# Kernel optimization log

Hardware: AMD Instinct MI355X
Metric: run time of the kernel (lower is better)

Reference implementation:

```python
import jax, jax.numpy as jnp
import numpy as np

B, N, C = 16, 1024, 1024
H = 16            # num_attention_heads
D = C // H        # attention_head_size = 64

def setup_inputs() -> dict:
    key = jax.random.key(0)
    k1, k2, k3 = jax.random.split(key, 3)
    scale = 1.0 / np.sqrt(C)
    return {
        "hidden_states": jax.random.normal(k1, (B, N, C), dtype=jnp.float32),
        "qkv_w": jax.random.normal(k2, (C, 3 * C), dtype=jnp.float32) * scale,
        "qkv_b": jnp.zeros((3 * C,), dtype=jnp.float32),
        "proj_w": jax.random.normal(k3, (C, C), dtype=jnp.float32) * scale,
        "proj_b": jnp.zeros((C,), dtype=jnp.float32),
    }

def reference(hidden_states, qkv_w, qkv_b, proj_w, proj_b):
    # fused QKV projection: [B, N, 3C]
    qkv = hidden_states @ qkv_w + qkv_b
    # reshape to [3, B, H, N, D]
    qkv = qkv.reshape(B, N, 3, H, D).transpose(2, 0, 3, 1, 4)
    q, k, v = qkv[0], qkv[1], qkv[2]
    # attention scores [B, H, N, N]
    scores = jnp.einsum("bhnd,bhmd->bhnm", q, k) / jnp.sqrt(jnp.float32(D))
    probs = jax.nn.softmax(scores, axis=-1)  # dropout_p=0 -> identity
    ctx = jnp.einsum("bhnm,bhmd->bhnd", probs, v)
    ctx = ctx.transpose(0, 2, 1, 3).reshape(B, N, C)
    # output projection
    return ctx @ proj_w + proj_b
```

## Files before the change

kernel.cpp:

```cpp
#include <hip/hip_runtime.h>


#define BB 16
#define NN 1024
#define CC 1024
#define HH 16
#define DD 64
#define BN (BB * NN)
#define HEADELEMS (256 * 1024 * 64)

typedef float  f4     __attribute__((ext_vector_type(4)));
typedef __bf16 bf16x8 __attribute__((ext_vector_type(8)));
typedef __bf16 bf16x4 __attribute__((ext_vector_type(4)));
typedef short  s8v    __attribute__((ext_vector_type(8)));
typedef short  s4v    __attribute__((ext_vector_type(4)));
typedef short  s2v    __attribute__((ext_vector_type(2)));

__device__ __forceinline__ short f2bf(float x) {
  union { float f; unsigned u; } a; a.f = x;
  unsigned r = a.u + 0x7fffu + ((a.u >> 16) & 1u);
  return (short)(r >> 16);
}

__device__ __forceinline__ void gl_lds16(const void* g, void* l) {
  __builtin_amdgcn_global_load_lds((__attribute__((address_space(1))) void*)g,
                                   (__attribute__((address_space(3))) void*)l,
                                   16, 0, 0);
}

__device__ __forceinline__ f4 mfma16(bf16x8 a, bf16x8 b, f4 c) {
  return __builtin_amdgcn_mfma_f32_16x16x32_bf16(a, b, c, 0, 0, 0);
}

__global__ void cast_bf16(const float* __restrict__ x, short* __restrict__ y) {
  int i = (blockIdx.x * 256 + threadIdx.x) * 4;
  float4 v = *(const float4*)&x[i];
  s4v o;
  o[0] = f2bf(v.x); o[1] = f2bf(v.y); o[2] = f2bf(v.z); o[3] = f2bf(v.w);
  *(s4v*)&y[i] = o;
}

__global__ void transpose_cast(const float* __restrict__ W, short* __restrict__ Wt,
                               int K, int Nw) {
  __shared__ float tile[32][33];
  int bx = blockIdx.x, by = blockIdx.y;
  int t = threadIdx.x;
  int tc = t & 31, tr = t >> 5;
#pragma unroll
  for (int i = 0; i < 4; ++i) {
    int r = tr + i * 8;
    tile[r][tc] = W[(size_t)(by * 32 + r) * Nw + bx * 32 + tc];
  }
  __syncthreads();
#pragma unroll
  for (int i = 0; i < 4; ++i) {
    int r = tr + i * 8;
    Wt[(size_t)(bx * 32 + r) * K + by * 32 + tc] = f2bf(tile[tc][r]);
  }
}

__global__ void transpose_v(const short* __restrict__ Vm, short* __restrict__ Vt) {
  __shared__ short tile[64][68];
  int bh = blockIdx.x, n0 = blockIdx.y * 64;
  const short* src = Vm + (size_t)bh * (NN * DD) + (size_t)n0 * DD;
  short* dst = Vt + (size_t)bh * (NN * DD) + n0;
  int t = threadIdx.x;
#pragma unroll
  for (int i2 = 0; i2 < 2; ++i2) {
    int i = t + i2 * 256;
    int r = i >> 3, c = i & 7;
    *(s8v*)&tile[r][c * 8] = *(const s8v*)&src[(size_t)r * DD + c * 8];
  }
  __syncthreads();
#pragma unroll
  for (int i2 = 0; i2 < 2; ++i2) {
    int i = t + i2 * 256;
    int d = i >> 3, c = i & 7;
    s8v v;
#pragma unroll
    for (int j = 0; j < 8; ++j) v[j] = tile[c * 8 + j][d];
    *(s8v*)&dst[(size_t)d * NN + c * 8] = v;
  }
}

template <int EPI>
__global__ __launch_bounds__(256, 2)
void gemm_bt(const short* __restrict__ A, const short* __restrict__ Bt,
             const float* __restrict__ bias, float* __restrict__ Cf,
             short* __restrict__ Cq, int M, int N, int K) {
  __shared__ short la[128 * 64];
  __shared__ short lb[128 * 64];
  const int t = threadIdx.x, lane = t & 63, w = t >> 6;
  const int row0 = blockIdx.y * 128, col0 = blockIdx.x * 128;
  const int wm = (w & 1) * 64, wn = (w >> 1) * 64;
  const int q = lane >> 4, ln = lane & 15;
  const int sr8 = lane >> 3;
  const int sc8 = (lane & 7) ^ sr8;
  f4 acc[4][4] = {};

  for (int kb = 0; kb < K; kb += 64) {
    __syncthreads();
#pragma unroll
    for (int rblk = 0; rblk < 4; ++rblk) {
      int rbase = (w * 4 + rblk) * 8;
      const short* ga = A + (size_t)(row0 + rbase + sr8) * K + kb + sc8 * 8;
      const short* gb = Bt + (size_t)(col0 + rbase + sr8) * K + kb + sc8 * 8;
      gl_lds16(ga, &la[rbase * 64]);
      gl_lds16(gb, &lb[rbase * 64]);
    }
    __syncthreads();
#pragma unroll
    for (int ks2 = 0; ks2 < 2; ++ks2) {
      const int c8 = ks2 * 4 + q;
      const int sw = (c8 ^ (ln & 7)) * 8;
      bf16x8 af[4], bfr[4];
#pragma unroll
      for (int i = 0; i < 4; ++i) {
        af[i]  = *(const bf16x8*)&la[(wm + i * 16 + ln) * 64 + sw];
        bfr[i] = *(const bf16x8*)&lb[(wn + i * 16 + ln) * 64 + sw];
      }
#pragma unroll
      for (int i = 0; i < 4; ++i)
#pragma unroll
        for (int j = 0; j < 4; ++j)
          acc[i][j] = mfma16(af[i], bfr[j], acc[i][j]);
    }
  }

#pragma unroll
  for (int i = 0; i < 4; ++i) {
    int rbase = row0 + wm + i * 16 + q * 4;
#pragma unroll
    for (int j = 0; j < 4; ++j) {
      int col = col0 + wn + j * 16 + ln;
      float bv = bias[col];
      if (EPI == 0) {
#pragma unroll
        for (int r2 = 0; r2 < 4; ++r2)
          Cf[(size_t)(rbase + r2) * N + col] = acc[i][j][r2] + bv;
      } else {
        int which = col >> 10, c = col & 1023;
        int h = c >> 6, d = c & 63;
        float scale = (which == 0) ? 0.1803368801f : 1.0f;
#pragma unroll
        for (int r2 = 0; r2 < 4; ++r2) {
          int row = rbase + r2;
          int bh = (row >> 10) * HH + h;
          size_t idx = ((size_t)bh * NN + (row & 1023)) * DD + d;
          Cq[(size_t)which * HEADELEMS + idx] = f2bf((acc[i][j][r2] + bv) * scale);
        }
      }
    }
  }
}

__global__ __launch_bounds__(512, 4)
void attn(const short* __restrict__ Qg, const short* __restrict__ Kg,
          const short* __restrict__ Vtg, short* __restrict__ ctx) {
  __shared__ short sQP[128 * 64];
  __shared__ short sK[2][64 * 64];
  __shared__ short sV[2][64 * 64];
  const int t = threadIdx.x, lane = t & 63, w = t >> 6;
  const int bh = blockIdx.x, qb = blockIdx.y;
  const short* Qh = Qg + (size_t)bh * (NN * DD) + qb * 128 * DD;
  const short* Kh = Kg + (size_t)bh * (NN * DD);
  const short* Vh = Vtg + (size_t)bh * (NN * DD);

  {
    int r0 = t >> 3, c0 = t & 7;
    gl_lds16(Qh + r0 * DD + ((c0 ^ (r0 & 7)) * 8), &sQP[t * 8]);
    int i1 = t + 512;
    int r1 = i1 >> 3, c1 = i1 & 7;
    gl_lds16(Qh + r1 * DD + ((c1 ^ (r1 & 7)) * 8), &sQP[i1 * 8]);
  }
  const int sr = t >> 3, sc = t & 7;
  const int ssc = ((sc ^ (sr & 7)) * 8);
  gl_lds16(Kh + sr * DD + ssc, &sK[0][t * 8]);
  gl_lds16(Vh + (size_t)sr * NN + ssc, &sV[0][t * 8]);

  __syncthreads();

  const int q = lane >> 4, ln = lane & 15;
  const int wq = w * 16;
  const int sw = ln & 7;

  bf16x8 qf[2];
  qf[0] = *(const bf16x8*)&sQP[(wq + ln) * 64 + ((0 + q) ^ sw) * 8];
  qf[1] = *(const bf16x8*)&sQP[(wq + ln) * 64 + ((4 + q) ^ sw) * 8];

  f4 o[4] = {};
  float lsum = 0.f;

  for (int kt = 0; kt < 16; ++kt) {
    const int cur = kt & 1;
    if (kt < 15) {
      const int nb = cur ^ 1;
      gl_lds16(Kh + (kt + 1) * 64 * DD + sr * DD + ssc, &sK[nb][t * 8]);
      gl_lds16(Vh + (size_t)sr * NN + (kt + 1) * 64 + ssc, &sV[nb][t * 8]);
    }

    f4 s[4] = {};
    __builtin_amdgcn_s_setprio(1);
#pragma unroll
    for (int ks = 0; ks < 2; ++ks) {
#pragma unroll
      for (int ki = 0; ki < 4; ++ki) {
        bf16x8 kf = *(const bf16x8*)&sK[cur][(ki * 16 + ln) * 64 + (((ks * 4 + q) ^ sw) * 8)];
        s[ki] = mfma16(kf, qf[ks], s[ki]);
      }
    }
    __builtin_amdgcn_s_setprio(0);

#pragma unroll
    for (int ki = 0; ki < 4; ++ki) {
      float p0 = exp2f(s[ki][0]), p1 = exp2f(s[ki][1]);
      float p2 = exp2f(s[ki][2]), p3 = exp2f(s[ki][3]);
      lsum += (p0 + p1) + (p2 + p3);
      bf16x4 pk;
      pk[0] = (__bf16)p0; pk[1] = (__bf16)p1;
      pk[2] = (__bf16)p2; pk[3] = (__bf16)p3;
      *(bf16x4*)&sQP[(wq + ln) * 64 + (((2 * ki + (q >> 1)) ^ sw) * 8) + (q & 1) * 4] = pk;
    }

    __builtin_amdgcn_s_setprio(1);
#pragma unroll
    for (int ks = 0; ks < 2; ++ks) {
      bf16x8 pf = *(const bf16x8*)&sQP[(wq + ln) * 64 + (((ks * 4 + q) ^ sw) * 8)];
#pragma unroll
      for (int j = 0; j < 4; ++j) {
        bf16x8 vf = *(const bf16x8*)&sV[cur][(j * 16 + ln) * 64 + (((ks * 4 + q) ^ sw) * 8)];
        o[j] = mfma16(pf, vf, o[j]);
      }
    }
    __builtin_amdgcn_s_setprio(0);

    __syncthreads();
  }

  float lfull = lsum;
  lfull += __shfl_xor(lfull, 16);
  lfull += __shfl_xor(lfull, 32);

#pragma unroll
  for (int r = 0; r < 4; ++r) {
    float lr = __shfl(lfull, q * 4 + r);
    float inv = 1.0f / lr;
    int token_row = qb * 128 + wq + q * 4 + r;
    size_t base = ((size_t)(bh >> 4) * NN + token_row) * CC + (bh & 15) * DD;
#pragma unroll
    for (int j = 0; j < 4; ++j)
      ctx[base + j * 16 + ln] = f2bf(o[j][r] * inv);
  }
}

extern "C" void kernel_launch(void* const* d_in, const int* in_sizes, int n_in,
                              void* d_out, int out_size, void* d_ws, size_t ws_size,
                              hipStream_t stream) {
  const float* hs     = (const float*)d_in[0];
  const float* qkv_w  = (const float*)d_in[1];
  const float* qkv_b  = (const float*)d_in[2];
  const float* proj_w = (const float*)d_in[3];
  const float* proj_b = (const float*)d_in[4];

  short* ws = (short*)d_ws;
  if (ws_size < 176160768ull) return;
  short* Xbf = ws;
  short* Wq  = ws + 16777216;
  short* Wp  = ws + 19922944;
  short* Qm  = ws + 20971520;
  short* Km  = ws + 37748736;
  short* Vm  = ws + 54525952;
  short* Ctx = ws + 71303168;
  short* Vt  = Xbf;

  cast_bf16<<<16384, 256, 0, stream>>>(hs, Xbf);
  transpose_cast<<<dim3(96, 32), 256, 0, stream>>>(qkv_w, Wq, 1024, 3072);
  transpose_cast<<<dim3(32, 32), 256, 0, stream>>>(proj_w, Wp, 1024, 1024);

  gemm_bt<1><<<dim3(24, 128), 256, 0, stream>>>(Xbf, Wq, qkv_b, nullptr, Qm,
                                                BN, 3 * CC, CC);
  transpose_v<<<dim3(256, 16), 256, 0, stream>>>(Vm, Vt);
  attn<<<dim3(256, 8), 512, 0, stream>>>(Qm, Km, Vt, Ctx);
  gemm_bt<0><<<dim3(8, 128), 256, 0, stream>>>(Ctx, Wp, proj_b, (float*)d_out, nullptr,
                                               BN, CC, CC);
}
```

Baseline: 420.8 us.

## Double-buffer GEMM, fuse V transpose into QKV epilogue, widen attention tiles

Measured after the change: 393.6 us. 1.07x faster.

```diff
diff --git a/kernel.cpp b/kernel.cpp
--- a/kernel.cpp
+++ b/kernel.cpp
@@ -16,6 +16,12 @@
 typedef short  s4v    __attribute__((ext_vector_type(4)));
 typedef short  s2v    __attribute__((ext_vector_type(2)));
 
+#if __has_builtin(__builtin_amdgcn_exp2f)
+#define EXP2(x) __builtin_amdgcn_exp2f(x)
+#else
+#define EXP2(x) exp2f(x)
+#endif
+
 __device__ __forceinline__ short f2bf(float x) {
   union { float f; unsigned u; } a; a.f = x;
   unsigned r = a.u + 0x7fffu + ((a.u >> 16) & 1u);
@@ -59,65 +65,51 @@
   }
 }
 
-__global__ void transpose_v(const short* __restrict__ Vm, short* __restrict__ Vt) {
-  __shared__ short tile[64][68];
-  int bh = blockIdx.x, n0 = blockIdx.y * 64;
-  const short* src = Vm + (size_t)bh * (NN * DD) + (size_t)n0 * DD;
-  short* dst = Vt + (size_t)bh * (NN * DD) + n0;
-  int t = threadIdx.x;
-#pragma unroll
-  for (int i2 = 0; i2 < 2; ++i2) {
-    int i = t + i2 * 256;
-    int r = i >> 3, c = i & 7;
-    *(s8v*)&tile[r][c * 8] = *(const s8v*)&src[(size_t)r * DD + c * 8];
-  }
-  __syncthreads();
-#pragma unroll
-  for (int i2 = 0; i2 < 2; ++i2) {
-    int i = t + i2 * 256;
-    int d = i >> 3, c = i & 7;
-    s8v v;
-#pragma unroll
-    for (int j = 0; j < 8; ++j) v[j] = tile[c * 8 + j][d];
-    *(s8v*)&dst[(size_t)d * NN + c * 8] = v;
-  }
-}
+#define GSTAGE(buf, kb)                                                        \
+  {                                                                            \
+    _Pragma("unroll")                                                          \
+    for (int rblk = 0; rblk < 4; ++rblk) {                                     \
+      int rbase = (w * 4 + rblk) * 8;                                          \
+      gl_lds16(A + (size_t)(row0 + rbase + sr8) * K + (kb) + sc8 * 8,          \
+               &la[buf][rbase * 64]);                                          \
+      gl_lds16(Bt + (size_t)(col0 + rbase + sr8) * K + (kb) + sc8 * 8,         \
+               &lb[buf][rbase * 64]);                                          \
+    }                                                                          \
+  }
 
 template <int EPI>
 __global__ __launch_bounds__(256, 2)
 void gemm_bt(const short* __restrict__ A, const short* __restrict__ Bt,
              const float* __restrict__ bias, float* __restrict__ Cf,
              short* __restrict__ Cq, int M, int N, int K) {
-  __shared__ short la[128 * 64];
-  __shared__ short lb[128 * 64];
+  __shared__ short la[2][128 * 64];
+  __shared__ short lb[2][128 * 64];
   const int t = threadIdx.x, lane = t & 63, w = t >> 6;
-  const int row0 = blockIdx.y * 128, col0 = blockIdx.x * 128;
+  int bid = blockIdx.y * gridDim.x + blockIdx.x;
+  int xcd = bid & 7, sub = bid >> 3;
+  int xg = sub >> 7, rem = sub & 127;
+  int xb = xg * 8 + (rem & 7), yb = xcd * 16 + (rem >> 3);
+  const int row0 = yb * 128, col0 = xb * 128;
   const int wm = (w & 1) * 64, wn = (w >> 1) * 64;
   const int q = lane >> 4, ln = lane & 15;
   const int sr8 = lane >> 3;
   const int sc8 = (lane & 7) ^ sr8;
   f4 acc[4][4] = {};
 
-  for (int kb = 0; kb < K; kb += 64) {
-    __syncthreads();
-#pragma unroll
-    for (int rblk = 0; rblk < 4; ++rblk) {
-      int rbase = (w * 4 + rblk) * 8;
-      const short* ga = A + (size_t)(row0 + rbase + sr8) * K + kb + sc8 * 8;
-      const short* gb = Bt + (size_t)(col0 + rbase + sr8) * K + kb + sc8 * 8;
-      gl_lds16(ga, &la[rbase * 64]);
-      gl_lds16(gb, &lb[rbase * 64]);
-    }
-    __syncthreads();
+  GSTAGE(0, 0);
+  __syncthreads();
+  int cur = 0;
+  for (int kb = 0; kb < K; kb += 64, cur ^= 1) {
+    if (kb + 64 < K) GSTAGE(cur ^ 1, kb + 64);
 #pragma unroll
     for (int ks2 = 0; ks2 < 2; ++ks2) {
       const int c8 = ks2 * 4 + q;
-      const int sw = (c8 ^ (ln & 7)) * 8;
+      const int swz = (c8 ^ (ln & 7)) * 8;
       bf16x8 af[4], bfr[4];
 #pragma unroll
       for (int i = 0; i < 4; ++i) {
-        af[i]  = *(const bf16x8*)&la[(wm + i * 16 + ln) * 64 + sw];
-        bfr[i] = *(const bf16x8*)&lb[(wn + i * 16 + ln) * 64 + sw];
+        af[i]  = *(const bf16x8*)&la[cur][(wm + i * 16 + ln) * 64 + swz];
+        bfr[i] = *(const bf16x8*)&lb[cur][(wn + i * 16 + ln) * 64 + swz];
       }
 #pragma unroll
       for (int i = 0; i < 4; ++i)
@@ -125,6 +117,7 @@
         for (int j = 0; j < 4; ++j)
           acc[i][j] = mfma16(af[i], bfr[j], acc[i][j]);
     }
+    __syncthreads();
   }
 
 #pragma unroll
@@ -141,13 +134,21 @@
       } else {
         int which = col >> 10, c = col & 1023;
         int h = c >> 6, d = c & 63;
-        float scale = (which == 0) ? 0.1803368801f : 1.0f;
-#pragma unroll
-        for (int r2 = 0; r2 < 4; ++r2) {
-          int row = rbase + r2;
-          int bh = (row >> 10) * HH + h;
-          size_t idx = ((size_t)bh * NN + (row & 1023)) * DD + d;
-          Cq[(size_t)which * HEADELEMS + idx] = f2bf((acc[i][j][r2] + bv) * scale);
+        if (which == 2) {
+          int bh = (rbase >> 10) * HH + h;
+          s4v vv;
+#pragma unroll
+          for (int r2 = 0; r2 < 4; ++r2) vv[r2] = f2bf(acc[i][j][r2] + bv);
+          *(s4v*)&Cq[(size_t)2 * HEADELEMS + ((size_t)bh * DD + d) * NN + (rbase & 1023)] = vv;
+        } else {
+          float scale = (which == 0) ? 0.1803368801f : 1.0f;
+#pragma unroll
+          for (int r2 = 0; r2 < 4; ++r2) {
+            int row = rbase + r2;
+            int bh = (row >> 10) * HH + h;
+            size_t idx = ((size_t)bh * NN + (row & 1023)) * DD + d;
+            Cq[(size_t)which * HEADELEMS + idx] = f2bf((acc[i][j][r2] + bv) * scale);
+          }
         }
       }
     }
@@ -157,21 +158,20 @@
 __global__ __launch_bounds__(512, 4)
 void attn(const short* __restrict__ Qg, const short* __restrict__ Kg,
           const short* __restrict__ Vtg, short* __restrict__ ctx) {
-  __shared__ short sQP[128 * 64];
+  __shared__ short sQP[256 * 64];
   __shared__ short sK[2][64 * 64];
   __shared__ short sV[2][64 * 64];
   const int t = threadIdx.x, lane = t & 63, w = t >> 6;
   const int bh = blockIdx.x, qb = blockIdx.y;
-  const short* Qh = Qg + (size_t)bh * (NN * DD) + qb * 128 * DD;
+  const short* Qh = Qg + (size_t)bh * (NN * DD) + qb * 256 * DD;
   const short* Kh = Kg + (size_t)bh * (NN * DD);
   const short* Vh = Vtg + (size_t)bh * (NN * DD);
 
-  {
-    int r0 = t >> 3, c0 = t & 7;
-    gl_lds16(Qh + r0 * DD + ((c0 ^ (r0 & 7)) * 8), &sQP[t * 8]);
-    int i1 = t + 512;
-    int r1 = i1 >> 3, c1 = i1 & 7;
-    gl_lds16(Qh + r1 * DD + ((c1 ^ (r1 & 7)) * 8), &sQP[i1 * 8]);
+#pragma unroll
+  for (int k = 0; k < 4; ++k) {
+    int i = t + k * 512;
+    int r = i >> 3, c = i & 7;
+    gl_lds16(Qh + r * DD + ((c ^ (r & 7)) * 8), &sQP[i * 8]);
   }
   const int sr = t >> 3, sc = t & 7;
   const int ssc = ((sc ^ (sr & 7)) * 8);
@@ -181,15 +181,18 @@
   __syncthreads();
 
   const int q = lane >> 4, ln = lane & 15;
-  const int wq = w * 16;
+  const int wq = w * 32;
   const int sw = ln & 7;
 
-  bf16x8 qf[2];
-  qf[0] = *(const bf16x8*)&sQP[(wq + ln) * 64 + ((0 + q) ^ sw) * 8];
-  qf[1] = *(const bf16x8*)&sQP[(wq + ln) * 64 + ((4 + q) ^ sw) * 8];
-
-  f4 o[4] = {};
-  float lsum = 0.f;
+  bf16x8 qf[2][2];
+#pragma unroll
+  for (int ks = 0; ks < 2; ++ks)
+#pragma unroll
+    for (int g = 0; g < 2; ++g)
+      qf[ks][g] = *(const bf16x8*)&sQP[(wq + g * 16 + ln) * 64 + (((ks * 4 + q) ^ sw) * 8)];
+
+  f4 o[2][4] = {};
+  float lsum0 = 0.f, lsum1 = 0.f;
 
   for (int kt = 0; kt < 16; ++kt) {
     const int cur = kt & 1;
@@ -199,37 +202,47 @@
       gl_lds16(Vh + (size_t)sr * NN + (kt + 1) * 64 + ssc, &sV[nb][t * 8]);
     }
 
-    f4 s[4] = {};
+    f4 s[4][2] = {};
     __builtin_amdgcn_s_setprio(1);
 #pragma unroll
-    for (int ks = 0; ks < 2; ++ks) {
+    for (int ks = 0; ks < 2; ++ks)
 #pragma unroll
       for (int ki = 0; ki < 4; ++ki) {
         bf16x8 kf = *(const bf16x8*)&sK[cur][(ki * 16 + ln) * 64 + (((ks * 4 + q) ^ sw) * 8)];
-        s[ki] = mfma16(kf, qf[ks], s[ki]);
-      }
-    }
+        s[ki][0] = mfma16(kf, qf[ks][0], s[ki][0]);
+        s[ki][1] = mfma16(kf, qf[ks][1], s[ki][1]);
+      }
     __builtin_amdgcn_s_setprio(0);
 
 #pragma unroll
-    for (int ki = 0; ki < 4; ++ki) {
-      float p0 = exp2f(s[ki][0]), p1 = exp2f(s[ki][1]);
-      float p2 = exp2f(s[ki][2]), p3 = exp2f(s[ki][3]);
-      lsum += (p0 + p1) + (p2 + p3);
-      bf16x4 pk;
-      pk[0] = (__bf16)p0; pk[1] = (__bf16)p1;
-      pk[2] = (__bf16)p2; pk[3] = (__bf16)p3;
-      *(bf16x4*)&sQP[(wq + ln) * 64 + (((2 * ki + (q >> 1)) ^ sw) * 8) + (q & 1) * 4] = pk;
-    }
+    for (int g = 0; g < 2; ++g)
+#pragma unroll
+      for (int ki = 0; ki < 4; ++ki) {
+        f4 sv = s[ki][g];
+        float p0 = EXP2(sv[0]), p1 = EXP2(sv[1]);
+        float p2 = EXP2(sv[2]), p3 = EXP2(sv[3]);
+        if (g == 0) lsum0 += (p0 + p1) + (p2 + p3);
+        else        lsum1 += (p0 + p1) + (p2 + p3);
+        bf16x4 pk;
+        pk[0] = (__bf16)p0; pk[1] = (__bf16)p1;
+        pk[2] = (__bf16)p2; pk[3] = (__bf16)p3;
+        *(bf16x4*)&sQP[(wq + g * 16 + ln) * 64 +
+                       (((2 * ki + (q >> 1)) ^ sw) * 8) + (q & 1) * 4] = pk;
+      }
 
     __builtin_amdgcn_s_setprio(1);
 #pragma unroll
     for (int ks = 0; ks < 2; ++ks) {
-      bf16x8 pf = *(const bf16x8*)&sQP[(wq + ln) * 64 + (((ks * 4 + q) ^ sw) * 8)];
-#pragma unroll
-      for (int j = 0; j < 4; ++j) {
-        bf16x8 vf = *(const bf16x8*)&sV[cur][(j * 16 + ln) * 64 + (((ks * 4 + q) ^ sw) * 8)];
-        o[j] = mfma16(pf, vf, o[j]);
+      bf16x8 vf[4];
+#pragma unroll
+      for (int j = 0; j < 4; ++j)
+        vf[j] = *(const bf16x8*)&sV[cur][(j * 16 + ln) * 64 + (((ks * 4 + q) ^ sw) * 8)];
+#pragma unroll
+      for (int g = 0; g < 2; ++g) {
+        bf16x8 pf = *(const bf16x8*)&sQP[(wq + g * 16 + ln) * 64 + (((ks * 4 + q) ^ sw) * 8)];
+#pragma unroll
+        for (int j = 0; j < 4; ++j)
+          o[g][j] = mfma16(pf, vf[j], o[g][j]);
       }
     }
     __builtin_amdgcn_s_setprio(0);
@@ -237,19 +250,21 @@
     __syncthreads();
   }
 
-  float lfull = lsum;
-  lfull += __shfl_xor(lfull, 16);
-  lfull += __shfl_xor(lfull, 32);
-
-#pragma unroll
-  for (int r = 0; r < 4; ++r) {
-    float lr = __shfl(lfull, q * 4 + r);
-    float inv = 1.0f / lr;
-    int token_row = qb * 128 + wq + q * 4 + r;
-    size_t base = ((size_t)(bh >> 4) * NN + token_row) * CC + (bh & 15) * DD;
-#pragma unroll
-    for (int j = 0; j < 4; ++j)
-      ctx[base + j * 16 + ln] = f2bf(o[j][r] * inv);
+#pragma unroll
+  for (int g = 0; g < 2; ++g) {
+    float lfull = (g == 0) ? lsum0 : lsum1;
+    lfull += __shfl_xor(lfull, 16);
+    lfull += __shfl_xor(lfull, 32);
+#pragma unroll
+    for (int r = 0; r < 4; ++r) {
+      float lr = __shfl(lfull, q * 4 + r);
+      float inv = 1.0f / lr;
+      int token_row = qb * 256 + wq + g * 16 + q * 4 + r;
+      size_t base = ((size_t)(bh >> 4) * NN + token_row) * CC + (bh & 15) * DD;
+#pragma unroll
+      for (int j = 0; j < 4; ++j)
+        ctx[base + j * 16 + ln] = f2bf(o[g][j][r] * inv);
+    }
   }
 }
 
@@ -269,9 +284,8 @@
   short* Wp  = ws + 19922944;
   short* Qm  = ws + 20971520;
   short* Km  = ws + 37748736;
-  short* Vm  = ws + 54525952;
+  short* Vt  = ws + 54525952;
   short* Ctx = ws + 71303168;
-  short* Vt  = Xbf;
 
   cast_bf16<<<16384, 256, 0, stream>>>(hs, Xbf);
   transpose_cast<<<dim3(96, 32), 256, 0, stream>>>(qkv_w, Wq, 1024, 3072);
@@ -279,8 +293,7 @@
 
   gemm_bt<1><<<dim3(24, 128), 256, 0, stream>>>(Xbf, Wq, qkv_b, nullptr, Qm,
                                                 BN, 3 * CC, CC);
-  transpose_v<<<dim3(256, 16), 256, 0, stream>>>(Vm, Vt);
-  attn<<<dim3(256, 8), 512, 0, stream>>>(Qm, Km, Vt, Ctx);
+  attn<<<dim3(256, 4), 512, 0, stream>>>(Qm, Km, Vt, Ctx);
   gemm_bt<0><<<dim3(8, 128), 256, 0, stream>>>(Ctx, Wp, proj_b, (float*)d_out, nullptr,
                                                BN, CC, CC);
 }
```
